# Kernel tuning notes

Measured on AMD Instinct MI355X. Metric: run time of the kernel, lower is better.

The kernel has to match this reference:

```python
import jax, jax.numpy as jnp
import numpy as np

B, F, H, N, S, L, E = 32, 128, 256, 2048, 3, 2, 262144
DEG = E // (B * N)  # average degree used to normalize position updates


def setup_inputs() -> dict:
    key = jax.random.key(0)
    ks = jax.random.split(key, 12)
    s = 0.05
    return {
        "x": jax.random.normal(ks[0], (B, F), jnp.float32),
        "positions": jax.random.normal(ks[1], (N, S), jnp.float32),
        "W_in": jax.random.normal(ks[2], (F, H), jnp.float32) * s,
        "b_in": jnp.zeros((H,), jnp.float32),
        "Wg1": jax.random.normal(ks[3], (3, H // 2), jnp.float32) * s,
        "bg1": jnp.zeros((H // 2,), jnp.float32),
        "Wg2": jax.random.normal(ks[4], (H // 2, H), jnp.float32) * s,
        "bg2": jnp.zeros((H,), jnp.float32),
        "Wm": jax.random.normal(ks[5], (L, 2 * H + 1, H), jnp.float32) * s,
        "bm": jnp.zeros((L, H), jnp.float32),
        "Wu": jax.random.normal(ks[6], (L, 2 * H, H), jnp.float32) * s,
        "bu": jnp.zeros((L, H), jnp.float32),
        "Wp": jax.random.normal(ks[7], (L, H, 1), jnp.float32) * s,
        "W_out": jax.random.normal(ks[8], (H, 1), jnp.float32) * s,
        "b_out": jnp.zeros((1,), jnp.float32),
        "edge_index": jax.random.randint(ks[9], (2, E), 0, B * N, dtype=jnp.int32),
    }


def _geometric_features(positions, Wg1, bg1, Wg2, bg2):
    # For single points, pairwise / centroid / Hausdorff distances all reduce to
    # the euclidean distance, so feature[i, 0..2] = mean_{j != i} ||p_i - p_j||.
    n = positions.shape[0]
    diff = positions[:, None, :] - positions[None, :, :]      # [N, N, S]
    dsq = jnp.sum(diff * diff, axis=-1)                        # [N, N]
    mask = 1.0 - jnp.eye(n, dtype=positions.dtype)
    d = jnp.sqrt(jnp.where(mask > 0, dsq, 1.0)) * mask         # grad-safe sqrt
    mean_d = jnp.sum(d, axis=1) / (n - 1)                      # [N]
    gf = jnp.stack([mean_d, mean_d, mean_d], axis=-1)          # [N, 3]
    return jax.nn.relu(gf @ Wg1 + bg1) @ Wg2 + bg2             # [N, H]


def _forward(x, positions, W_in, b_in, Wg1, bg1, Wg2, bg2, Wm, bm, Wu, bu, Wp, W_out, b_out, edge_index):
    nn_ = B * N
    h = x @ W_in + b_in                                        # [B, H]
    h = jnp.broadcast_to(h[:, None, :], (B, N, H)).reshape(nn_, H)
    pos = jnp.broadcast_to(positions[None], (B, N, S)).reshape(nn_, S)
    g = _geometric_features(positions, Wg1, bg1, Wg2, bg2)     # [N, H]
    h = h + jnp.broadcast_to(g[None], (B, N, H)).reshape(nn_, H)
    src, dst = edge_index[0], edge_index[1]
    for l in range(L):  # small fixed layer loop
        dvec = pos[src] - pos[dst]
        d = jnp.sqrt(jnp.sum(dvec * dvec, axis=-1, keepdims=True) + 1e-12)  # [E, 1]
        m = jax.nn.relu(jnp.concatenate([h[src], h[dst], d], axis=-1) @ Wm[l] + bm[l])
        agg = jax.ops.segment_sum(m, dst, num_segments=nn_)    # [B*N, H]
        coef = m @ Wp[l]                                       # [E, 1]
        pos = pos + jax.ops.segment_sum((pos[dst] - pos[src]) * coef, dst, num_segments=nn_) / DEG
        h = h + jax.nn.relu(jnp.concatenate([h, agg], axis=-1) @ Wu[l] + bu[l])
    out = (h.reshape(B, N, H) @ W_out + b_out).squeeze(-1)     # [B, N]
    return out


def reference(x, positions, W_in, b_in, Wg1, bg1, Wg2, bg2, Wm, bm, Wu, bu, Wp, W_out, b_out, edge_index):
    return _forward(x, positions, W_in, b_in, Wg1, bg1, Wg2, bg2, Wm, bm, Wu, bu, Wp, W_out, b_out, edge_index)
```

## Files before the change

kernel.cpp:

```cpp
#include <hip/hip_runtime.h>
#include <math.h>

#define B_ 32
#define F_ 128
#define H_ 256
#define N_ 2048
#define L_ 2
#define E_ 262144
#define NN_ 65536

typedef __attribute__((ext_vector_type(8))) short short8;
typedef __attribute__((ext_vector_type(4))) float f32x4;
typedef __attribute__((ext_vector_type(2))) float f32x2;

static __device__ __forceinline__ unsigned short f2bf(float f) {
  unsigned int u = __float_as_uint(f);
  u += 0x7FFF + ((u >> 16) & 1);
  return (unsigned short)(u >> 16);
}
static __device__ __forceinline__ float bf2f(unsigned short u) {
  return __uint_as_float(((unsigned int)u) << 16);
}
static __device__ __forceinline__ unsigned int pk_bf16(float lo, float hi) {
  unsigned int r;
  asm("v_cvt_pk_bf16_f32 %0, %1, %2" : "=v"(r) : "v"(lo), "v"(hi));
  return r;
}

typedef const __attribute__((address_space(1))) unsigned int* as1p;
typedef __attribute__((address_space(3))) unsigned int* as3p;
static __device__ __forceinline__ void gload16(const void* g, void* l) {
  __builtin_amdgcn_global_load_lds((as1p)g, (as3p)l, 16, 0, 0);
}
#define VMCNT0() asm volatile("s_waitcnt vmcnt(0)" ::: "memory")


__global__ void h0_kernel(const float* __restrict__ x, const float* __restrict__ W_in,
                          const float* __restrict__ b_in, float* __restrict__ h0) {
  int b = blockIdx.x;
  int j = threadIdx.x;
  float acc = b_in[j];
#pragma unroll 8
  for (int k = 0; k < F_; ++k)
    acc += x[b * F_ + k] * W_in[k * H_ + j];
  h0[b * H_ + j] = acc;
}

__global__ void meand_g_kernel(const float* __restrict__ positions,
                               const float* __restrict__ Wg1, const float* __restrict__ bg1,
                               const float* __restrict__ Wg2, const float* __restrict__ bg2,
                               float* __restrict__ g) {
  __shared__ float red[256];
  __shared__ float hid[128];
  int n = blockIdx.x;
  int t = threadIdx.x;
  float px = positions[n * 3 + 0], py = positions[n * 3 + 1], pz = positions[n * 3 + 2];
  float s = 0.f;
  for (int j = t; j < N_; j += 256) {
    float dx = px - positions[j * 3 + 0];
    float dy = py - positions[j * 3 + 1];
    float dz = pz - positions[j * 3 + 2];
    s += sqrtf(dx * dx + dy * dy + dz * dz);
  }
  red[t] = s;
  __syncthreads();
  for (int off = 128; off > 0; off >>= 1) {
    if (t < off) red[t] += red[t + off];
    __syncthreads();
  }
  float md = red[0] / (float)(N_ - 1);
  if (t < 128) {
    float w = Wg1[t] + Wg1[128 + t] + Wg1[256 + t];
    hid[t] = fmaxf(md * w + bg1[t], 0.f);
  }
  __syncthreads();
  float acc = bg2[t];
#pragma unroll 8
  for (int k = 0; k < 128; ++k)
    acc += hid[k] * Wg2[k * H_ + t];
  g[n * H_ + t] = acc;
}

__global__ void hbfinit_kernel(const float* __restrict__ h0, const float* __restrict__ g,
                               unsigned short* __restrict__ hbf) {
  int idx = blockIdx.x * blockDim.x + threadIdx.x;
  int row = idx >> 5;
  int c8 = (idx & 31) << 3;
  const float* hp = h0 + (row >> 11) * H_ + c8;
  const float* gp = g + (row & (N_ - 1)) * H_ + c8;
  const float4 a = *(const float4*)hp;
  const float4 a2 = *(const float4*)(hp + 4);
  const float4 b = *(const float4*)gp;
  const float4 b2 = *(const float4*)(gp + 4);
  short8 v;
  v[0] = (short)f2bf(a.x + b.x);  v[1] = (short)f2bf(a.y + b.y);
  v[2] = (short)f2bf(a.z + b.z);  v[3] = (short)f2bf(a.w + b.w);
  v[4] = (short)f2bf(a2.x + b2.x); v[5] = (short)f2bf(a2.y + b2.y);
  v[6] = (short)f2bf(a2.z + b2.z); v[7] = (short)f2bf(a2.w + b2.w);
  *(short8*)(hbf + (((size_t)row) << 8) + c8) = v;
}

__global__ void posinit_kernel(const float* __restrict__ positions, float* __restrict__ pos4) {
  int n = blockIdx.x * blockDim.x + threadIdx.x;
  int src = (n & (N_ - 1)) * 3;
  float4 v;
  v.x = positions[src + 0];
  v.y = positions[src + 1];
  v.z = positions[src + 2];
  v.w = 0.f;
  *(float4*)(pos4 + ((size_t)n << 2)) = v;
}


__global__ void deg_kernel(const int* __restrict__ ei, int* __restrict__ deg) {
  int e = blockIdx.x * 256 + threadIdx.x;
  atomicAdd(&deg[ei[E_ + e]], 1);
}

__global__ void scan1_kernel(const int* __restrict__ deg, int* __restrict__ bsum) {
  __shared__ int red[256];
  int t = threadIdx.x;
  red[t] = deg[blockIdx.x * 256 + t];
  __syncthreads();
  for (int off = 128; off > 0; off >>= 1) {
    if (t < off) red[t] += red[t + off];
    __syncthreads();
  }
  if (t == 0) bsum[blockIdx.x] = red[0];
}

__global__ void scan2_kernel(int* __restrict__ bsum) {
  __shared__ int s[256];
  int t = threadIdx.x;
  s[t] = bsum[t];
  __syncthreads();
  for (int off = 1; off < 256; off <<= 1) {
    int v = (t >= off) ? s[t - off] : 0;
    __syncthreads();
    s[t] += v;
    __syncthreads();
  }
  bsum[t] = (t == 0) ? 0 : s[t - 1];
}

__global__ void scan3_kernel(const int* __restrict__ deg, const int* __restrict__ bsum,
                             int* __restrict__ cur, int* __restrict__ rowptr) {
  __shared__ int s[256];
  int t = threadIdx.x;
  int i = blockIdx.x * 256 + t;
  s[t] = deg[i];
  __syncthreads();
  for (int off = 1; off < 256; off <<= 1) {
    int v = (t >= off) ? s[t - off] : 0;
    __syncthreads();
    s[t] += v;
    __syncthreads();
  }
  int excl = (t == 0) ? 0 : s[t - 1];
  int v = bsum[blockIdx.x] + excl;
  cur[i] = v;
  rowptr[i] = v;
}

__global__ void scatter_kernel(const int* __restrict__ ei, int* __restrict__ cur,
                               int* __restrict__ src_s) {
  int e = blockIdx.x * 256 + threadIdx.x;
  int s = ei[e], d = ei[E_ + e];
  int p = atomicAdd(&cur[d], 1);
  src_s[p] = s;
}

__global__ void wconv_all(const float* __restrict__ Wm, const float* __restrict__ Wu,
                          unsigned short* __restrict__ Wt1, unsigned short* __restrict__ Wut) {
  int idx = blockIdx.x * 256 + threadIdx.x;
  int sel = idx >> 14;
  int rem = idx & 16383;
  if (sel < 2) {
    const float* W = Wm + (size_t)sel * 513 * H_;
    unsigned short* dst = Wt1 + (size_t)sel * 131072 + ((size_t)rem << 3);
    int g = rem >> 13;
    int r2 = rem & 8191;
    int kc = r2 >> 11, w = (r2 >> 9) & 3, ks = (r2 >> 8) & 1, ni = (r2 >> 6) & 3, lane = r2 & 63;
    int r = lane & 15, q = lane >> 4;
    int n  = (w << 6) + (ni << 4) + r;
    int kb = (g << 8) + (kc << 6) + (ks << 5) + (q << 3);
#pragma unroll
    for (int j = 0; j < 8; ++j)
      dst[j] = f2bf(W[(size_t)(kb + j) * H_ + n]);
  } else {
    const float* W = Wu + (size_t)(sel - 2) * 512 * H_;
    unsigned short* dst = Wut + (size_t)(sel - 2) * 131072 + ((size_t)rem << 3);
    int kc = rem >> 11, w = (rem >> 9) & 3, ks = (rem >> 8) & 1, ni = (rem >> 6) & 3, lane = rem & 63;
    int r = lane & 15, q = lane >> 4;
    int n  = (w << 6) + (ni << 4) + r;
    int kb = (kc << 6) + (ks << 5) + (q << 3);
#pragma unroll
    for (int j = 0; j < 8; ++j)
      dst[j] = f2bf(W[(size_t)(kb + j) * H_ + n]);
  }
}


#define GEMM_IDS                                                     \
  const int t = threadIdx.x;                                         \
  const int m0 = blockIdx.x << 6;                                    \
  const int wu = __builtin_amdgcn_readfirstlane(t >> 6);             \
  const int lane = t & 63;                                           \
  const int q = lane >> 4;                                           \
  const int r = lane & 15;                                           \
  const int l8 = lane >> 3;                                          \
  const int sq = (lane & 7) ^ l8;

#define STAGE_PHASE(abase, colb, wsrc_base, bb)                                         \
  do {                                                                                  \
    _Pragma("unroll")                                                                   \
    for (int i_ = 0; i_ < 2; ++i_) {                                                    \
      const int Rl_ = (wu << 4) + (i_ << 3) + l8;                                       \
      gload16((abase) + (((size_t)(m0 + Rl_)) << 8) + (colb) + (sq << 3),               \
              &sA[bb][((wu << 4) + (i_ << 3)) << 6]);                                   \
    }                                                                                   \
    _Pragma("unroll")                                                                   \
    for (int j_ = 0; j_ < 8; ++j_) {                                                    \
      gload16((wsrc_base) + (wu << 12) + (j_ << 9) + (lane << 3),                       \
              &sB[bb][(wu << 12) + (j_ << 9)]);                                         \
    }                                                                                   \
  } while (0)

#define COMPUTE_PHASE(bb)                                                               \
  do {                                                                                  \
    _Pragma("unroll")                                                                   \
    for (int ks = 0; ks < 2; ++ks) {                                                    \
      short8 af[4], bfr[4];                                                             \
      _Pragma("unroll")                                                                 \
      for (int mi = 0; mi < 4; ++mi)                                                    \
        af[mi] = *(const short8*)(&sA[bb][((mi * 16 + r) << 6) +                        \
                                          ((((ks << 2) + q) ^ (r & 7)) << 3)]);        \
      _Pragma("unroll")                                                                 \
      for (int ni = 0; ni < 4; ++ni)                                                    \
        bfr[ni] = *(const short8*)(&sB[bb][(wu << 12) + (ks << 11) + (ni << 9) +        \
                                           (lane << 3)]);                               \
      _Pragma("unroll")                                                                 \
      for (int mi = 0; mi < 4; ++mi)                                                    \
        _Pragma("unroll")                                                               \
        for (int ni = 0; ni < 4; ++ni)                                                  \
          acc[mi][ni] =                                                                 \
              __builtin_amdgcn_mfma_f32_16x16x32_bf16(af[mi], bfr[ni], acc[mi][ni],     \
                                                      0, 0, 0);                         \
    }                                                                                   \
  } while (0)

__launch_bounds__(256)
__global__ void gemm1_mfma(const unsigned short* __restrict__ hbf,
                           const unsigned short* __restrict__ Wt,
                           const float* __restrict__ bm,
                           unsigned short* __restrict__ X, unsigned short* __restrict__ Zb) {
  __shared__ __align__(16) unsigned short sA[2][4096];
  __shared__ __align__(16) unsigned short sB[2][16384];
  GEMM_IDS

  f32x4 acc[4][4];
#pragma unroll
  for (int mi = 0; mi < 4; ++mi)
#pragma unroll
    for (int ni = 0; ni < 4; ++ni)
      acc[mi][ni] = (f32x4){0.f, 0.f, 0.f, 0.f};

  STAGE_PHASE(hbf, 0, Wt, 0);
  VMCNT0();
  __syncthreads();

  int buf = 0;
  for (int p = 0; p < 8; ++p) {
    if (p < 7)
      STAGE_PHASE(hbf, ((p + 1) & 3) << 6, Wt + ((size_t)(p + 1) << 14), buf ^ 1);
    COMPUTE_PHASE(buf);
    if (p == 3) {
#pragma unroll
      for (int ni = 0; ni < 4; ++ni) {
        int n = (wu << 6) + ni * 16 + r;
#pragma unroll
        for (int mi = 0; mi < 4; ++mi)
#pragma unroll
          for (int reg = 0; reg < 4; ++reg) {
            size_t idx = (((size_t)(m0 + mi * 16 + q * 4 + reg)) << 8) + n;
            X[idx] = f2bf(acc[mi][ni][reg]);
            acc[mi][ni][reg] = 0.f;
          }
      }
    }
    if (p < 7) {
      VMCNT0();
      __syncthreads();
      buf ^= 1;
    }
  }

#pragma unroll
  for (int ni = 0; ni < 4; ++ni) {
    int n = (wu << 6) + ni * 16 + r;
    float bmn = bm[n];
#pragma unroll
    for (int mi = 0; mi < 4; ++mi)
#pragma unroll
      for (int reg = 0; reg < 4; ++reg) {
        size_t idx = (((size_t)(m0 + mi * 16 + q * 4 + reg)) << 8) + n;
        Zb[idx] = f2bf(acc[mi][ni][reg] + bmn);
      }
  }
}

static __device__ __forceinline__ void edge_do(
    const float4 pn, const float4 q, const uint2 xv,
    const f32x2 z01, const f32x2 z23,
    const f32x2 wl01, const f32x2 wl23,
    const f32x2 wp01, const f32x2 wp23,
    f32x2& a01, f32x2& a23,
    float& pdx, float& pdy, float& pdz) {
  const float dx = pn.x - q.x, dy = pn.y - q.y, dz = pn.z - q.z;
  const float d = sqrtf(dx * dx + dy * dy + dz * dz + 1e-12f);
  f32x2 dd; dd[0] = d; dd[1] = d;
  f32x2 x01, x23;
  x01[0] = __uint_as_float(xv.x << 16);
  x01[1] = __uint_as_float(xv.x & 0xffff0000u);
  x23[0] = __uint_as_float(xv.y << 16);
  x23[1] = __uint_as_float(xv.y & 0xffff0000u);
  f32x2 v01 = x01 + z01 + dd * wl01;
  f32x2 v23 = x23 + z23 + dd * wl23;
  v01[0] = fmaxf(v01[0], 0.f); v01[1] = fmaxf(v01[1], 0.f);
  v23[0] = fmaxf(v23[0], 0.f); v23[1] = fmaxf(v23[1], 0.f);
  a01 += v01; a23 += v23;
  const f32x2 cpv = v01 * wp01 + v23 * wp23;
  const float cp = cpv[0] + cpv[1];
  pdx += dx * cp; pdy += dy * cp; pdz += dz * cp;
}

__launch_bounds__(256)
__global__ void edge_kernel(const unsigned short* __restrict__ X,
                            const unsigned short* __restrict__ Zb,
                            const float* __restrict__ pos_c,
                            const int* __restrict__ rowptr, const int* __restrict__ src_s,
                            const float* __restrict__ wl, const float* __restrict__ wp,
                            unsigned short* __restrict__ aggb, float* __restrict__ pos_o) {
  const int gid = blockIdx.x * 256 + threadIdx.x;
  const int n = __builtin_amdgcn_readfirstlane(gid >> 6);
  const int lane = threadIdx.x & 63;

  const float4 wlv = *(const float4*)(wl + (lane << 2));
  const float4 wpv = *(const float4*)(wp + (lane << 2));
  const f32x2 wl01 = {wlv.x, wlv.y}, wl23 = {wlv.z, wlv.w};
  const f32x2 wp01 = {wpv.x, wpv.y}, wp23 = {wpv.z, wpv.w};

  const int e0 = rowptr[n];
  const int e1 = (n == NN_ - 1) ? E_ : rowptr[n + 1];

  const uint2 zv = *(const uint2*)(Zb + (((size_t)n) << 8) + (lane << 2));
  f32x2 z01, z23;
  z01[0] = __uint_as_float(zv.x << 16);
  z01[1] = __uint_as_float(zv.x & 0xffff0000u);
  z23[0] = __uint_as_float(zv.y << 16);
  z23[1] = __uint_as_float(zv.y & 0xffff0000u);

  const float4 pn = *(const float4*)(pos_c + ((size_t)n << 2));
  f32x2 a01 = {0.f, 0.f}, a23 = {0.f, 0.f};
  float pdx = 0.f, pdy = 0.f, pdz = 0.f;

  const unsigned short* Xl = X + (lane << 2);

  int e = e0;
  for (; e + 4 <= e1; e += 4) {
    const int s0 = src_s[e], s1 = src_s[e + 1], s2 = src_s[e + 2], s3 = src_s[e + 3];
    const float4 q0 = *(const float4*)(pos_c + ((size_t)s0 << 2));
    const float4 q1 = *(const float4*)(pos_c + ((size_t)s1 << 2));
    const float4 q2 = *(const float4*)(pos_c + ((size_t)s2 << 2));
    const float4 q3 = *(const float4*)(pos_c + ((size_t)s3 << 2));
    const uint2 x0 = *(const uint2*)(Xl + (((size_t)s0) << 8));
    const uint2 x1 = *(const uint2*)(Xl + (((size_t)s1) << 8));
    const uint2 x2 = *(const uint2*)(Xl + (((size_t)s2) << 8));
    const uint2 x3 = *(const uint2*)(Xl + (((size_t)s3) << 8));
    edge_do(pn, q0, x0, z01, z23, wl01, wl23, wp01, wp23, a01, a23, pdx, pdy, pdz);
    edge_do(pn, q1, x1, z01, z23, wl01, wl23, wp01, wp23, a01, a23, pdx, pdy, pdz);
    edge_do(pn, q2, x2, z01, z23, wl01, wl23, wp01, wp23, a01, a23, pdx, pdy, pdz);
    edge_do(pn, q3, x3, z01, z23, wl01, wl23, wp01, wp23, a01, a23, pdx, pdy, pdz);
  }
  if (e + 2 <= e1) {
    const int s0 = src_s[e], s1 = src_s[e + 1];
    const float4 q0 = *(const float4*)(pos_c + ((size_t)s0 << 2));
    const float4 q1 = *(const float4*)(pos_c + ((size_t)s1 << 2));
    const uint2 x0 = *(const uint2*)(Xl + (((size_t)s0) << 8));
    const uint2 x1 = *(const uint2*)(Xl + (((size_t)s1) << 8));
    edge_do(pn, q0, x0, z01, z23, wl01, wl23, wp01, wp23, a01, a23, pdx, pdy, pdz);
    edge_do(pn, q1, x1, z01, z23, wl01, wl23, wp01, wp23, a01, a23, pdx, pdy, pdz);
    e += 2;
  }
  if (e < e1) {
    const int s0 = src_s[e];
    const float4 q0 = *(const float4*)(pos_c + ((size_t)s0 << 2));
    const uint2 x0 = *(const uint2*)(Xl + (((size_t)s0) << 8));
    edge_do(pn, q0, x0, z01, z23, wl01, wl23, wp01, wp23, a01, a23, pdx, pdy, pdz);
  }

  uint2 av;
  av.x = pk_bf16(a01[0], a01[1]);
  av.y = pk_bf16(a23[0], a23[1]);
  *(uint2*)(aggb + (((size_t)n) << 8) + (lane << 2)) = av;

#pragma unroll
  for (int m = 1; m < 64; m <<= 1) {
    pdx += __shfl_xor(pdx, m, 64);
    pdy += __shfl_xor(pdy, m, 64);
    pdz += __shfl_xor(pdz, m, 64);
  }
  if (lane == 0) {
    float4 po;
    po.x = pn.x + pdx * 0.25f;
    po.y = pn.y + pdy * 0.25f;
    po.z = pn.z + pdz * 0.25f;
    po.w = 0.f;
    *(float4*)(pos_o + ((size_t)n << 2)) = po;
  }
}

__launch_bounds__(256)
__global__ void upd2_mfma(unsigned short* __restrict__ hbf,
                          const unsigned short* __restrict__ aggb,
                          const unsigned short* __restrict__ Wt,
                          const float* __restrict__ bu) {
  __shared__ __align__(16) unsigned short sA[2][4096];
  __shared__ __align__(16) unsigned short sB[2][16384];
  GEMM_IDS

  f32x4 acc[4][4];
#pragma unroll
  for (int mi = 0; mi < 4; ++mi)
#pragma unroll
    for (int ni = 0; ni < 4; ++ni)
      acc[mi][ni] = (f32x4){0.f, 0.f, 0.f, 0.f};

  STAGE_PHASE(hbf, 0, Wt, 0);
  VMCNT0();
  __syncthreads();

  int buf = 0;
  for (int p = 0; p < 8; ++p) {
    if (p < 7) {
      const unsigned short* ab = (p + 1 < 4) ? hbf : aggb;
      STAGE_PHASE(ab, ((p + 1) & 3) << 6, Wt + ((size_t)(p + 1) << 14), buf ^ 1);
    }
    COMPUTE_PHASE(buf);
    if (p < 7) {
      VMCNT0();
      __syncthreads();
      buf ^= 1;
    }
  }

#pragma unroll
  for (int ni = 0; ni < 4; ++ni) {
    int n = (wu << 6) + ni * 16 + r;
    float buv = bu[n];
#pragma unroll
    for (int mi = 0; mi < 4; ++mi)
#pragma unroll
      for (int reg = 0; reg < 4; ++reg) {
        size_t idx = (((size_t)(m0 + mi * 16 + q * 4 + reg)) << 8) + n;
        float v = bf2f(hbf[idx]) + fmaxf(acc[mi][ni][reg] + buv, 0.f);
        hbf[idx] = f2bf(v);
      }
  }
}

__launch_bounds__(256)
__global__ void upd2_out(const unsigned short* __restrict__ hbf,
                         const unsigned short* __restrict__ aggb,
                         const unsigned short* __restrict__ Wt,
                         const float* __restrict__ bu,
                         const float* __restrict__ Wout, const float* __restrict__ bout,
                         float* __restrict__ out) {
  __shared__ __align__(16) unsigned short sA[2][4096];
  __shared__ __align__(16) unsigned short sB[2][16384];
  GEMM_IDS

  f32x4 acc[4][4];
#pragma unroll
  for (int mi = 0; mi < 4; ++mi)
#pragma unroll
    for (int ni = 0; ni < 4; ++ni)
      acc[mi][ni] = (f32x4){0.f, 0.f, 0.f, 0.f};

  STAGE_PHASE(hbf, 0, Wt, 0);
  VMCNT0();
  __syncthreads();

  int buf = 0;
  for (int p = 0; p < 8; ++p) {
    if (p < 7) {
      const unsigned short* ab = (p + 1 < 4) ? hbf : aggb;
      STAGE_PHASE(ab, ((p + 1) & 3) << 6, Wt + ((size_t)(p + 1) << 14), buf ^ 1);
    }
    COMPUTE_PHASE(buf);
    if (p < 7) {
      VMCNT0();
      __syncthreads();
      buf ^= 1;
    }
  }
  __syncthreads();
  float (*sRed)[64] = (float(*)[64])(&sA[0][0]);

  float dotp[4][4];
#pragma unroll
  for (int mi = 0; mi < 4; ++mi)
#pragma unroll
    for (int reg = 0; reg < 4; ++reg)
      dotp[mi][reg] = 0.f;

#pragma unroll
  for (int ni = 0; ni < 4; ++ni) {
    int n = (wu << 6) + ni * 16 + r;
    float buv = bu[n];
    float won = Wout[n];
#pragma unroll
    for (int mi = 0; mi < 4; ++mi)
#pragma unroll
      for (int reg = 0; reg < 4; ++reg) {
        size_t idx = (((size_t)(m0 + mi * 16 + q * 4 + reg)) << 8) + n;
        float v = bf2f(hbf[idx]) + fmaxf(acc[mi][ni][reg] + buv, 0.f);
        dotp[mi][reg] += v * won;
      }
  }
#pragma unroll
  for (int mask = 1; mask < 16; mask <<= 1)
#pragma unroll
    for (int mi = 0; mi < 4; ++mi)
#pragma unroll
      for (int reg = 0; reg < 4; ++reg)
        dotp[mi][reg] += __shfl_xor(dotp[mi][reg], mask, 64);
  if (r == 0) {
#pragma unroll
    for (int mi = 0; mi < 4; ++mi)
#pragma unroll
      for (int reg = 0; reg < 4; ++reg)
        sRed[wu][mi * 16 + q * 4 + reg] = dotp[mi][reg];
  }
  __syncthreads();
  if (t < 64)
    out[m0 + t] = sRed[0][t] + sRed[1][t] + sRed[2][t] + sRed[3][t] + bout[0];
}


extern "C" void kernel_launch(void* const* d_in, const int* in_sizes, int n_in,
                              void* d_out, int out_size, void* d_ws, size_t ws_size,
                              hipStream_t stream) {
  const float* x         = (const float*)d_in[0];
  const float* positions = (const float*)d_in[1];
  const float* W_in      = (const float*)d_in[2];
  const float* b_in      = (const float*)d_in[3];
  const float* Wg1       = (const float*)d_in[4];
  const float* bg1       = (const float*)d_in[5];
  const float* Wg2       = (const float*)d_in[6];
  const float* bg2       = (const float*)d_in[7];
  const float* Wm        = (const float*)d_in[8];
  const float* bm        = (const float*)d_in[9];
  const float* Wu        = (const float*)d_in[10];
  const float* bu        = (const float*)d_in[11];
  const float* Wp        = (const float*)d_in[12];
  const float* W_out     = (const float*)d_in[13];
  const float* b_out     = (const float*)d_in[14];
  const int*   ei        = (const int*)d_in[15];
  float* out = (float*)d_out;

  char* ws = (char*)d_ws;
  unsigned short* hbf   = (unsigned short*)(ws);
  unsigned short* X     = (unsigned short*)(ws +  33554432UL);
  unsigned short* Zb    = (unsigned short*)(ws +  67108864UL);
  unsigned short* aggb  = (unsigned short*)(ws + 100663296UL);
  float*          posA  = (float*)(ws + 134217728UL);
  float*          posB  = (float*)(ws + 135266304UL);
  float*          g     = (float*)(ws + 136314880UL);
  float*          h0    = (float*)(ws + 138412032UL);
  unsigned short* Wt1   = (unsigned short*)(ws + 138444800UL);
  unsigned short* Wut   = (unsigned short*)(ws + 138969088UL);
  int*            deg   = (int*)(ws + 139493376UL);
  int*            cur   = (int*)(ws + 139755520UL);
  int*            bsum  = (int*)(ws + 140017664UL);
  int*            rowptr= (int*)(ws + 140018688UL);
  int*            src_s = (int*)(ws + 140280832UL);

  hipMemsetAsync(deg, 0, (size_t)NN_ * sizeof(int), stream);
  deg_kernel<<<E_ / 256, 256, 0, stream>>>(ei, deg);
  scan1_kernel<<<256, 256, 0, stream>>>(deg, bsum);
  scan2_kernel<<<1, 256, 0, stream>>>(bsum);
  scan3_kernel<<<256, 256, 0, stream>>>(deg, bsum, cur, rowptr);
  scatter_kernel<<<E_ / 256, 256, 0, stream>>>(ei, cur, src_s);

  wconv_all<<<256, 256, 0, stream>>>(Wm, Wu, Wt1, Wut);

  h0_kernel<<<B_, 256, 0, stream>>>(x, W_in, b_in, h0);
  meand_g_kernel<<<N_, 256, 0, stream>>>(positions, Wg1, bg1, Wg2, bg2, g);
  hbfinit_kernel<<<NN_ * 32 / 256, 256, 0, stream>>>(h0, g, hbf);
  posinit_kernel<<<NN_ / 256, 256, 0, stream>>>(positions, posA);

  float* pos_cur = posA;
  float* pos_nxt = posB;
  for (int l = 0; l < L_; ++l) {
    gemm1_mfma<<<NN_ / 64, 256, 0, stream>>>(hbf, Wt1 + (size_t)l * 131072,
                                             bm + (size_t)l * H_, X, Zb);
    edge_kernel<<<NN_ / 4, 256, 0, stream>>>(X, Zb, pos_cur, rowptr, src_s,
                                             Wm + (size_t)l * 513 * H_ + 512 * H_,
                                             Wp + (size_t)l * H_, aggb, pos_nxt);
    if (l < L_ - 1) {
      upd2_mfma<<<NN_ / 64, 256, 0, stream>>>(hbf, aggb, Wut + (size_t)l * 131072,
                                              bu + (size_t)l * H_);
    } else {
      upd2_out<<<NN_ / 64, 256, 0, stream>>>(hbf, aggb, Wut + (size_t)l * 131072,
                                             bu + (size_t)l * H_, W_out, b_out, out);
    }
    float* tmp = pos_cur; pos_cur = pos_nxt; pos_nxt = tmp;
  }
}
```

Measured before the change: 347.5 us.

## Deepen GEMM staging to 4-buffer, 3-ahead pipeline with partial vmcnt waits

The three MFMA GEMM kernels now split K into 16 phases of 32 instead of 8 phases of 64. They keep four LDS buffers with loads issued three phases ahead. Waits use partial vmcnt counts plus a raw barrier instead of a full drain each phase, so memory latency overlaps with MFMA compute. In exchange there are twice as many barriers, a new XOR swizzle for the smaller A tile, and more fragile hand-counted vmcnt values.

Result: faster. 333.7 us (-4.0%).

```diff
diff --git a/kernel.cpp b/kernel.cpp
--- a/kernel.cpp
+++ b/kernel.cpp
@@ -32,7 +32,6 @@
 static __device__ __forceinline__ void gload16(const void* g, void* l) {
   __builtin_amdgcn_global_load_lds((as1p)g, (as3p)l, 16, 0, 0);
 }
-#define VMCNT0() asm volatile("s_waitcnt vmcnt(0)" ::: "memory")
 
 
 __global__ void h0_kernel(const float* __restrict__ x, const float* __restrict__ W_in,
@@ -208,73 +207,74 @@
   const int lane = t & 63;                                           \
   const int q = lane >> 4;                                           \
   const int r = lane & 15;                                           \
-  const int l8 = lane >> 3;                                          \
-  const int sq = (lane & 7) ^ l8;
-
-#define STAGE_PHASE(abase, colb, wsrc_base, bb)                                         \
-  do {                                                                                  \
-    _Pragma("unroll")                                                                   \
-    for (int i_ = 0; i_ < 2; ++i_) {                                                    \
-      const int Rl_ = (wu << 4) + (i_ << 3) + l8;                                       \
-      gload16((abase) + (((size_t)(m0 + Rl_)) << 8) + (colb) + (sq << 3),               \
-              &sA[bb][((wu << 4) + (i_ << 3)) << 6]);                                   \
-    }                                                                                   \
-    _Pragma("unroll")                                                                   \
-    for (int j_ = 0; j_ < 8; ++j_) {                                                    \
-      gload16((wsrc_base) + (wu << 12) + (j_ << 9) + (lane << 3),                       \
-              &sB[bb][(wu << 12) + (j_ << 9)]);                                         \
-    }                                                                                   \
+  const int arow = lane >> 2;                                        \
+  const int aq = (lane & 3) ^ ((lane >> 2) & 3);
+
+#define STAGE_P(P, abase)                                                                \
+  do {                                                                                   \
+    gload16((abase) + (((size_t)(m0 + (wu << 4) + arow)) << 8) + (((P) & 7) << 5) +      \
+                (aq << 3),                                                               \
+            &sA[(P) & 3][wu << 9]);                                                      \
+    _Pragma("unroll")                                                                    \
+    for (int j_ = 0; j_ < 4; ++j_)                                                       \
+      gload16(Wt + (((size_t)((P) >> 1)) << 14) + (wu << 12) + (((P) & 1) << 11) +       \
+                  (j_ << 9) + (lane << 3),                                               \
+              &sB[(P) & 3][(wu << 11) + (j_ << 9)]);                                     \
   } while (0)
 
-#define COMPUTE_PHASE(bb)                                                               \
-  do {                                                                                  \
-    _Pragma("unroll")                                                                   \
-    for (int ks = 0; ks < 2; ++ks) {                                                    \
-      short8 af[4], bfr[4];                                                             \
-      _Pragma("unroll")                                                                 \
-      for (int mi = 0; mi < 4; ++mi)                                                    \
-        af[mi] = *(const short8*)(&sA[bb][((mi * 16 + r) << 6) +                        \
-                                          ((((ks << 2) + q) ^ (r & 7)) << 3)]);        \
-      _Pragma("unroll")                                                                 \
-      for (int ni = 0; ni < 4; ++ni)                                                    \
-        bfr[ni] = *(const short8*)(&sB[bb][(wu << 12) + (ks << 11) + (ni << 9) +        \
-                                           (lane << 3)]);                               \
-      _Pragma("unroll")                                                                 \
-      for (int mi = 0; mi < 4; ++mi)                                                    \
-        _Pragma("unroll")                                                               \
-        for (int ni = 0; ni < 4; ++ni)                                                  \
-          acc[mi][ni] =                                                                 \
-              __builtin_amdgcn_mfma_f32_16x16x32_bf16(af[mi], bfr[ni], acc[mi][ni],     \
-                                                      0, 0, 0);                         \
-    }                                                                                   \
+#define COMPUTE_P(P)                                                                     \
+  do {                                                                                   \
+    short8 af[4], bfr[4];                                                                \
+    _Pragma("unroll")                                                                    \
+    for (int mi = 0; mi < 4; ++mi)                                                       \
+      af[mi] = *(const short8*)(&sA[(P) & 3][((mi * 16 + r) << 5) +                      \
+                                             ((q ^ (r & 3)) << 3)]);                     \
+    _Pragma("unroll")                                                                    \
+    for (int ni = 0; ni < 4; ++ni)                                                       \
+      bfr[ni] = *(const short8*)(&sB[(P) & 3][(wu << 11) + (ni << 9) + (lane << 3)]);    \
+    _Pragma("unroll")                                                                    \
+    for (int mi = 0; mi < 4; ++mi)                                                       \
+      _Pragma("unroll")                                                                  \
+      for (int ni = 0; ni < 4; ++ni)                                                     \
+        acc[mi][ni] = __builtin_amdgcn_mfma_f32_16x16x32_bf16(af[mi], bfr[ni],           \
+                                                              acc[mi][ni], 0, 0, 0);     \
   } while (0)
+
+#define WAIT_BAR(P)                                                       \
+  do {                                                                    \
+    if ((P) <= 13)      asm volatile("s_waitcnt vmcnt(10)" ::: "memory"); \
+    else if ((P) == 14) asm volatile("s_waitcnt vmcnt(5)" ::: "memory");  \
+    else                asm volatile("s_waitcnt vmcnt(0)" ::: "memory");  \
+    __builtin_amdgcn_s_barrier();                                         \
+    asm volatile("" ::: "memory");                                        \
+  } while (0)
+
+#define ACC_ZERO()                                   \
+  _Pragma("unroll")                                  \
+  for (int mi = 0; mi < 4; ++mi)                     \
+    _Pragma("unroll")                                \
+    for (int ni = 0; ni < 4; ++ni)                   \
+      acc[mi][ni] = (f32x4){0.f, 0.f, 0.f, 0.f};
 
 __launch_bounds__(256)
 __global__ void gemm1_mfma(const unsigned short* __restrict__ hbf,
                            const unsigned short* __restrict__ Wt,
                            const float* __restrict__ bm,
                            unsigned short* __restrict__ X, unsigned short* __restrict__ Zb) {
-  __shared__ __align__(16) unsigned short sA[2][4096];
-  __shared__ __align__(16) unsigned short sB[2][16384];
+  __shared__ __align__(16) unsigned short sA[4][2048];
+  __shared__ __align__(16) unsigned short sB[4][8192];
   GEMM_IDS
 
   f32x4 acc[4][4];
-#pragma unroll
-  for (int mi = 0; mi < 4; ++mi)
-#pragma unroll
-    for (int ni = 0; ni < 4; ++ni)
-      acc[mi][ni] = (f32x4){0.f, 0.f, 0.f, 0.f};
-
-  STAGE_PHASE(hbf, 0, Wt, 0);
-  VMCNT0();
-  __syncthreads();
-
-  int buf = 0;
-  for (int p = 0; p < 8; ++p) {
-    if (p < 7)
-      STAGE_PHASE(hbf, ((p + 1) & 3) << 6, Wt + ((size_t)(p + 1) << 14), buf ^ 1);
-    COMPUTE_PHASE(buf);
-    if (p == 3) {
+  ACC_ZERO();
+
+  STAGE_P(0, hbf); STAGE_P(1, hbf); STAGE_P(2, hbf);
+#pragma unroll
+  for (int p = 0; p < 16; ++p) {
+    WAIT_BAR(p);
+    if (p + 3 < 16) STAGE_P(p + 3, hbf);
+    COMPUTE_P(p);
+    if (p == 7) {
 #pragma unroll
       for (int ni = 0; ni < 4; ++ni) {
         int n = (wu << 6) + ni * 16 + r;
@@ -287,11 +287,6 @@
             acc[mi][ni][reg] = 0.f;
           }
       }
-    }
-    if (p < 7) {
-      VMCNT0();
-      __syncthreads();
-      buf ^= 1;
     }
   }
 
@@ -425,33 +420,23 @@
                           const unsigned short* __restrict__ aggb,
                           const unsigned short* __restrict__ Wt,
                           const float* __restrict__ bu) {
-  __shared__ __align__(16) unsigned short sA[2][4096];
-  __shared__ __align__(16) unsigned short sB[2][16384];
+  __shared__ __align__(16) unsigned short sA[4][2048];
+  __shared__ __align__(16) unsigned short sB[4][8192];
   GEMM_IDS
 
   f32x4 acc[4][4];
-#pragma unroll
-  for (int mi = 0; mi < 4; ++mi)
-#pragma unroll
-    for (int ni = 0; ni < 4; ++ni)
-      acc[mi][ni] = (f32x4){0.f, 0.f, 0.f, 0.f};
-
-  STAGE_PHASE(hbf, 0, Wt, 0);
-  VMCNT0();
-  __syncthreads();
-
-  int buf = 0;
-  for (int p = 0; p < 8; ++p) {
-    if (p < 7) {
-      const unsigned short* ab = (p + 1 < 4) ? hbf : aggb;
-      STAGE_PHASE(ab, ((p + 1) & 3) << 6, Wt + ((size_t)(p + 1) << 14), buf ^ 1);
+  ACC_ZERO();
+
+  const unsigned short* hb = (const unsigned short*)hbf;
+  STAGE_P(0, hb); STAGE_P(1, hb); STAGE_P(2, hb);
+#pragma unroll
+  for (int p = 0; p < 16; ++p) {
+    WAIT_BAR(p);
+    if (p + 3 < 16) {
+      const unsigned short* ab = (p + 3 < 8) ? hb : aggb;
+      STAGE_P(p + 3, ab);
     }
-    COMPUTE_PHASE(buf);
-    if (p < 7) {
-      VMCNT0();
-      __syncthreads();
-      buf ^= 1;
-    }
+    COMPUTE_P(p);
   }
 
 #pragma unroll
@@ -476,33 +461,22 @@
                          const float* __restrict__ bu,
                          const float* __restrict__ Wout, const float* __restrict__ bout,
                          float* __restrict__ out) {
-  __shared__ __align__(16) unsigned short sA[2][4096];
-  __shared__ __align__(16) unsigned short sB[2][16384];
+  __shared__ __align__(16) unsigned short sA[4][2048];
+  __shared__ __align__(16) unsigned short sB[4][8192];
   GEMM_IDS
 
   f32x4 acc[4][4];
-#pragma unroll
-  for (int mi = 0; mi < 4; ++mi)
-#pragma unroll
-    for (int ni = 0; ni < 4; ++ni)
-      acc[mi][ni] = (f32x4){0.f, 0.f, 0.f, 0.f};
-
-  STAGE_PHASE(hbf, 0, Wt, 0);
-  VMCNT0();
-  __syncthreads();
-
-  int buf = 0;
-  for (int p = 0; p < 8; ++p) {
-    if (p < 7) {
-      const unsigned short* ab = (p + 1 < 4) ? hbf : aggb;
-      STAGE_PHASE(ab, ((p + 1) & 3) << 6, Wt + ((size_t)(p + 1) << 14), buf ^ 1);
+  ACC_ZERO();
+
+  STAGE_P(0, hbf); STAGE_P(1, hbf); STAGE_P(2, hbf);
+#pragma unroll
+  for (int p = 0; p < 16; ++p) {
+    WAIT_BAR(p);
+    if (p + 3 < 16) {
+      const unsigned short* ab = (p + 3 < 8) ? hbf : aggb;
+      STAGE_P(p + 3, ab);
     }
-    COMPUTE_PHASE(buf);
-    if (p < 7) {
-      VMCNT0();
-      __syncthreads();
-      buf ^= 1;
-    }
+    COMPUTE_P(p);
   }
   __syncthreads();
   float (*sRed)[64] = (float(*)[64])(&sA[0][0]);
```
